# Optimization experiments

Measured on AMD Instinct MI355X. Metric: run time of the kernel, lower is better.

## Reference

```python
import jax, jax.numpy as jnp
import numpy as np


def setup_inputs() -> dict:
    key = jax.random.key(0)
    ks = jax.random.split(key, 7)
    B = 65536
    x = jax.random.normal(ks[0], (B, 1, 28, 28), dtype=jnp.float32)
    conv_w = jax.random.normal(ks[1], (4, 1, 7, 7), dtype=jnp.float32) * 0.1
    conv_b = jax.random.normal(ks[2], (4,), dtype=jnp.float32) * 0.1
    fc1_w = jax.random.normal(ks[3], (64, 256), dtype=jnp.float32) * 0.05
    fc1_b = jax.random.normal(ks[4], (64,), dtype=jnp.float32) * 0.05
    fc2_w = jax.random.normal(ks[5], (10, 64), dtype=jnp.float32) * 0.1
    fc2_b = jax.random.normal(ks[6], (10,), dtype=jnp.float32) * 0.1
    return {"x": x, "conv_w": conv_w, "conv_b": conv_b,
            "fc1_w": fc1_w, "fc1_b": fc1_b, "fc2_w": fc2_w, "fc2_b": fc2_b}


def reference(x, conv_w, conv_b, fc1_w, fc1_b, fc2_w, fc2_b):
    # conv1: 1->4 channels, 7x7 kernel, stride 3, no padding -> [B,4,8,8]
    h = jax.lax.conv_general_dilated(
        x, conv_w, window_strides=(3, 3), padding="VALID",
        dimension_numbers=("NCHW", "OIHW", "NCHW"))
    h = h + conv_b[None, :, None, None]
    h = h * h  # SquareFunction (CKKS polynomial activation)
    h = h.reshape(h.shape[0], -1)  # [B, 256]
    h = jnp.einsum("bi,oi->bo", h, fc1_w) + fc1_b
    h = h * h  # SquareFunction
    out = jnp.einsum("bi,oi->bo", h, fc2_w) + fc2_b  # [B, 10]
    return out
```

## Files before the change

### kernel.cpp

```cpp
#include <hip/hip_runtime.h>


#define BLK_IMGS    64
#define CHUNK_IMGS  16
#define NCHUNK      4
#define XCH_FLOATS  (CHUNK_IMGS * 784)
#define HB_PITCH    65

#define LDS_XBUF    0
#define LDS_H       12544
#define LDS_H2      29184
#define LDS_W2      33280
#define LDS_OUT     34304
#define LDS_TOTAL_F 34944

__global__ __launch_bounds__(1024)
void encconv_fused5(const float* __restrict__ x,
                    const float* __restrict__ conv_w,
                    const float* __restrict__ conv_b,
                    const float* __restrict__ fc1_w,
                    const float* __restrict__ fc1_b,
                    const float* __restrict__ fc2_w,
                    const float* __restrict__ fc2_b,
                    float* __restrict__ out)
{
    extern __shared__ float lds[];
    float*  xbuf = lds + LDS_XBUF;
    float4* hb   = (float4*)(lds + LDS_H);
    float4* h2b  = (float4*)(lds + LDS_H2);
    float4* w2b  = (float4*)(lds + LDS_W2);
    float*  ob   = lds + LDS_OUT;

    const int tid  = threadIdx.x;
    const int blk  = blockIdx.x;
    const long base_img = (long)blk * BLK_IMGS;

    const int lane = tid & 63;
    const int c    = __builtin_amdgcn_readfirstlane((tid >> 6) & 3);
    const int ghi  = __builtin_amdgcn_readfirstlane(tid >> 8);
    const int glo  = lane >> 4;
    const int y    = (lane >> 1) & 7;
    const int xh   = lane & 1;
    const int g    = ghi * 4 + glo;

    float ws[49];
    #pragma unroll
    for (int i = 0; i < 49; ++i) ws[i] = conv_w[c * 49 + i];
    const float cb = conv_b[c];

    if (tid < 160) {
        float4 v = *(const float4*)(fc2_w + tid * 4);
        int e  = tid * 4;
        int j  = e >> 6;
        int kk = (e & 63) >> 2;
        w2b[kk * 16 + j] = v;
    }

    const float* xblk = x + base_img * 784;

    float4 pf0, pf1, pf2, pf3;
    {
        const float* src = xblk;
        pf0 = *(const float4*)(src + 4 * tid);
        pf1 = *(const float4*)(src + 4 * (tid + 1024));
        pf2 = *(const float4*)(src + 4 * (tid + 2048));
        if (tid < 64) pf3 = *(const float4*)(src + 4 * (tid + 3072));
    }

    for (int ch = 0; ch < NCHUNK; ++ch) {
        *(float4*)(xbuf + 4 * tid)          = pf0;
        *(float4*)(xbuf + 4 * (tid + 1024)) = pf1;
        *(float4*)(xbuf + 4 * (tid + 2048)) = pf2;
        if (tid < 64) *(float4*)(xbuf + 4 * (tid + 3072)) = pf3;
        __syncthreads();

        if (ch + 1 < NCHUNK) {
            const float* src = xblk + (ch + 1) * XCH_FLOATS;
            pf0 = *(const float4*)(src + 4 * tid);
            pf1 = *(const float4*)(src + 4 * (tid + 1024));
            pf2 = *(const float4*)(src + 4 * (tid + 2048));
            if (tid < 64) pf3 = *(const float4*)(src + 4 * (tid + 3072));
        }

        float acc0 = 0.f, acc1 = 0.f, acc2 = 0.f, acc3 = 0.f;
        const float* xi = xbuf + g * 784;
        #pragma unroll
        for (int rr = 0; rr < 7; ++rr) {
            const float* rp = xi + (3 * y + rr) * 28 + 12 * xh;
            float4 r0 = *(const float4*)(rp + 0);
            float4 r1 = *(const float4*)(rp + 4);
            float4 r2 = *(const float4*)(rp + 8);
            float4 r3 = *(const float4*)(rp + 12);
            float r[16] = { r0.x, r0.y, r0.z, r0.w,
                            r1.x, r1.y, r1.z, r1.w,
                            r2.x, r2.y, r2.z, r2.w,
                            r3.x, r3.y, r3.z, r3.w };
            #pragma unroll
            for (int kx = 0; kx < 7; ++kx) {
                const float w = ws[rr * 7 + kx];
                acc0 = fmaf(r[0 + kx], w, acc0);
                acc1 = fmaf(r[3 + kx], w, acc1);
                acc2 = fmaf(r[6 + kx], w, acc2);
                acc3 = fmaf(r[9 + kx], w, acc3);
            }
        }

        float4 hv;
        hv.x = acc0 + cb; hv.x *= hv.x;
        hv.y = acc1 + cb; hv.y *= hv.y;
        hv.z = acc2 + cb; hv.z *= hv.z;
        hv.w = acc3 + cb; hv.w *= hv.w;
        hb[(c * 16 + y * 2 + xh) * HB_PITCH + (ch * CHUNK_IMGS + g)] = hv;

        __syncthreads();
    }

    {
        const int img = tid & 63;
        const int w4  = __builtin_amdgcn_readfirstlane(tid >> 6);
        const float* wbase = fc1_w + (w4 * 4) * 256;

        float a0 = 0.f, a1 = 0.f, a2 = 0.f, a3 = 0.f;

        #pragma unroll 4
        for (int k4 = 0; k4 < 64; ++k4) {
            float4 h4 = hb[k4 * HB_PITCH + img];
            const float* wp = wbase + k4 * 4;
            float4 w0 = *(const float4*)(wp + 0 * 256);
            float4 w1 = *(const float4*)(wp + 1 * 256);
            float4 w2 = *(const float4*)(wp + 2 * 256);
            float4 w3 = *(const float4*)(wp + 3 * 256);
            a0 = fmaf(h4.x,w0.x,a0); a0 = fmaf(h4.y,w0.y,a0); a0 = fmaf(h4.z,w0.z,a0); a0 = fmaf(h4.w,w0.w,a0);
            a1 = fmaf(h4.x,w1.x,a1); a1 = fmaf(h4.y,w1.y,a1); a1 = fmaf(h4.z,w1.z,a1); a1 = fmaf(h4.w,w1.w,a1);
            a2 = fmaf(h4.x,w2.x,a2); a2 = fmaf(h4.y,w2.y,a2); a2 = fmaf(h4.z,w2.z,a2); a2 = fmaf(h4.w,w2.w,a2);
            a3 = fmaf(h4.x,w3.x,a3); a3 = fmaf(h4.y,w3.y,a3); a3 = fmaf(h4.z,w3.z,a3); a3 = fmaf(h4.w,w3.w,a3);
        }

        const float* bp = fc1_b + w4 * 4;
        float4 p0;
        p0.x = a0 + bp[0]; p0.x *= p0.x;
        p0.y = a1 + bp[1]; p0.y *= p0.y;
        p0.z = a2 + bp[2]; p0.z *= p0.z;
        p0.w = a3 + bp[3]; p0.w *= p0.w;
        h2b[w4 * 64 + img] = p0;
    }
    __syncthreads();

    if (tid < 512) {
        const int im3 = tid >> 3;
        const int q   = tid & 7;

        float s1 = 0.f;
        #pragma unroll
        for (int k4 = 0; k4 < 16; ++k4) {
            float4 hh = h2b[k4 * 64 + im3];
            float4 wA = w2b[k4 * 16 + q];
            s1 = fmaf(hh.x, wA.x, s1); s1 = fmaf(hh.y, wA.y, s1);
            s1 = fmaf(hh.z, wA.z, s1); s1 = fmaf(hh.w, wA.w, s1);
        }
        ob[im3 * 10 + q] = s1 + fc2_b[q];

        if (q < 2) {
            float s2 = 0.f;
            #pragma unroll
            for (int k4 = 0; k4 < 16; ++k4) {
                float4 hh = h2b[k4 * 64 + im3];
                float4 wB = w2b[k4 * 16 + 8 + q];
                s2 = fmaf(hh.x, wB.x, s2); s2 = fmaf(hh.y, wB.y, s2);
                s2 = fmaf(hh.z, wB.z, s2); s2 = fmaf(hh.w, wB.w, s2);
            }
            ob[im3 * 10 + 8 + q] = s2 + fc2_b[8 + q];
        }
    }
    __syncthreads();

    if (tid < 160) {
        float4 v = *(const float4*)(ob + tid * 4);
        *(float4*)(out + (long)blk * 640 + tid * 4) = v;
    }
}

extern "C" void kernel_launch(void* const* d_in, const int* in_sizes, int n_in,
                              void* d_out, int out_size, void* d_ws, size_t ws_size,
                              hipStream_t stream) {
    const float* x      = (const float*)d_in[0];
    const float* conv_w = (const float*)d_in[1];
    const float* conv_b = (const float*)d_in[2];
    const float* fc1_w  = (const float*)d_in[3];
    const float* fc1_b  = (const float*)d_in[4];
    const float* fc2_w  = (const float*)d_in[5];
    const float* fc2_b  = (const float*)d_in[6];
    float* out = (float*)d_out;

    const int B = in_sizes[0] / 784;
    const int blocks = (B + BLK_IMGS - 1) / BLK_IMGS;
    const size_t lds_bytes = LDS_TOTAL_F * sizeof(float);

    static bool attr_set = false;
    if (!attr_set) {
        (void)hipFuncSetAttribute((const void*)encconv_fused5,
                                  hipFuncAttributeMaxDynamicSharedMemorySize,
                                  (int)lds_bytes);
        attr_set = true;
    }

    encconv_fused5<<<blocks, 1024, lds_bytes, stream>>>(
        x, conv_w, conv_b, fc1_w, fc1_b, fc2_w, fc2_b, out);
}
```

Baseline: 342.5 us.

## Interleave per-chunk fc1/fc2 with conv and use LDS atomics for fc2

FC1 and FC2 now run per 16-image chunk inside the chunk loop, overlapping the previous chunk's dense layers with the next chunk's LDS fill. FC2 is done by each thread atomically adding its hidden unit's contribution into LDS outputs pre-initialised with the bias. The h buffer shrinks to one chunk, which roughly halves LDS use and could allow two blocks per CU. The cost is 10 LDS float atomics per thread per chunk and more redundant global reads of fc1_w, and atomic ordering makes float summation nondeterministic.

```diff
diff --git a/kernel.cpp b/kernel.cpp
--- a/kernel.cpp
+++ b/kernel.cpp
@@ -5,17 +5,15 @@
 #define CHUNK_IMGS  16
 #define NCHUNK      4
 #define XCH_FLOATS  (CHUNK_IMGS * 784)
-#define HB_PITCH    65
+#define HB_PITCH    17
 
 #define LDS_XBUF    0
 #define LDS_H       12544
-#define LDS_H2      29184
-#define LDS_W2      33280
-#define LDS_OUT     34304
-#define LDS_TOTAL_F 34944
+#define LDS_OUT     16896
+#define LDS_TOTAL_F 17536
 
 __global__ __launch_bounds__(1024)
-void encconv_fused5(const float* __restrict__ x,
+void encconv_fused6(const float* __restrict__ x,
                     const float* __restrict__ conv_w,
                     const float* __restrict__ conv_b,
                     const float* __restrict__ fc1_w,
@@ -27,8 +25,6 @@
     extern __shared__ float lds[];
     float*  xbuf = lds + LDS_XBUF;
     float4* hb   = (float4*)(lds + LDS_H);
-    float4* h2b  = (float4*)(lds + LDS_H2);
-    float4* w2b  = (float4*)(lds + LDS_W2);
     float*  ob   = lds + LDS_OUT;
 
     const int tid  = threadIdx.x;
@@ -48,13 +44,11 @@
     for (int i = 0; i < 49; ++i) ws[i] = conv_w[c * 49 + i];
     const float cb = conv_b[c];
 
-    if (tid < 160) {
-        float4 v = *(const float4*)(fc2_w + tid * 4);
-        int e  = tid * 4;
-        int j  = e >> 6;
-        int kk = (e & 63) >> 2;
-        w2b[kk * 16 + j] = v;
-    }
+    const int o_sub = (tid >> 4) & 3;
+    const int img16 = tid & 15;
+    const int o     = ((tid >> 6) << 2) + o_sub;
+
+    if (tid < 640) ob[tid] = fc2_b[tid % 10];
 
     const float* xblk = x + base_img * 784;
 
@@ -67,11 +61,32 @@
         if (tid < 64) pf3 = *(const float4*)(src + 4 * (tid + 3072));
     }
 
+    auto fc1fc2 = [&](int ch) {
+        const float* wrow = fc1_w + o * 256;
+        float acc = 0.f;
+        #pragma unroll 4
+        for (int k4 = 0; k4 < 64; ++k4) {
+            float4 h4 = hb[k4 * HB_PITCH + img16];
+            float4 w4 = *(const float4*)(wrow + k4 * 4);
+            acc = fmaf(h4.x, w4.x, acc); acc = fmaf(h4.y, w4.y, acc);
+            acc = fmaf(h4.z, w4.z, acc); acc = fmaf(h4.w, w4.w, acc);
+        }
+        float t  = acc + fc1_b[o];
+        float h2 = t * t;
+        const int ig = ch * CHUNK_IMGS + img16;
+        #pragma unroll
+        for (int j = 0; j < 10; ++j) {
+            atomicAdd(ob + ig * 10 + j, h2 * fc2_w[j * 64 + o]);
+        }
+    };
+
     for (int ch = 0; ch < NCHUNK; ++ch) {
         *(float4*)(xbuf + 4 * tid)          = pf0;
         *(float4*)(xbuf + 4 * (tid + 1024)) = pf1;
         *(float4*)(xbuf + 4 * (tid + 2048)) = pf2;
         if (tid < 64) *(float4*)(xbuf + 4 * (tid + 3072)) = pf3;
+
+        if (ch > 0) fc1fc2(ch - 1);
         __syncthreads();
 
         if (ch + 1 < NCHUNK) {
@@ -110,68 +125,12 @@
         hv.y = acc1 + cb; hv.y *= hv.y;
         hv.z = acc2 + cb; hv.z *= hv.z;
         hv.w = acc3 + cb; hv.w *= hv.w;
-        hb[(c * 16 + y * 2 + xh) * HB_PITCH + (ch * CHUNK_IMGS + g)] = hv;
+        hb[(c * 16 + y * 2 + xh) * HB_PITCH + g] = hv;
 
         __syncthreads();
     }
 
-    {
-        const int img = tid & 63;
-        const int w4  = __builtin_amdgcn_readfirstlane(tid >> 6);
-        const float* wbase = fc1_w + (w4 * 4) * 256;
-
-        float a0 = 0.f, a1 = 0.f, a2 = 0.f, a3 = 0.f;
-
-        #pragma unroll 4
-        for (int k4 = 0; k4 < 64; ++k4) {
-            float4 h4 = hb[k4 * HB_PITCH + img];
-            const float* wp = wbase + k4 * 4;
-            float4 w0 = *(const float4*)(wp + 0 * 256);
-            float4 w1 = *(const float4*)(wp + 1 * 256);
-            float4 w2 = *(const float4*)(wp + 2 * 256);
-            float4 w3 = *(const float4*)(wp + 3 * 256);
-            a0 = fmaf(h4.x,w0.x,a0); a0 = fmaf(h4.y,w0.y,a0); a0 = fmaf(h4.z,w0.z,a0); a0 = fmaf(h4.w,w0.w,a0);
-            a1 = fmaf(h4.x,w1.x,a1); a1 = fmaf(h4.y,w1.y,a1); a1 = fmaf(h4.z,w1.z,a1); a1 = fmaf(h4.w,w1.w,a1);
-            a2 = fmaf(h4.x,w2.x,a2); a2 = fmaf(h4.y,w2.y,a2); a2 = fmaf(h4.z,w2.z,a2); a2 = fmaf(h4.w,w2.w,a2);
-            a3 = fmaf(h4.x,w3.x,a3); a3 = fmaf(h4.y,w3.y,a3); a3 = fmaf(h4.z,w3.z,a3); a3 = fmaf(h4.w,w3.w,a3);
-        }
-
-        const float* bp = fc1_b + w4 * 4;
-        float4 p0;
-        p0.x = a0 + bp[0]; p0.x *= p0.x;
-        p0.y = a1 + bp[1]; p0.y *= p0.y;
-        p0.z = a2 + bp[2]; p0.z *= p0.z;
-        p0.w = a3 + bp[3]; p0.w *= p0.w;
-        h2b[w4 * 64 + img] = p0;
-    }
-    __syncthreads();
-
-    if (tid < 512) {
-        const int im3 = tid >> 3;
-        const int q   = tid & 7;
-
-        float s1 = 0.f;
-        #pragma unroll
-        for (int k4 = 0; k4 < 16; ++k4) {
-            float4 hh = h2b[k4 * 64 + im3];
-            float4 wA = w2b[k4 * 16 + q];
-            s1 = fmaf(hh.x, wA.x, s1); s1 = fmaf(hh.y, wA.y, s1);
-            s1 = fmaf(hh.z, wA.z, s1); s1 = fmaf(hh.w, wA.w, s1);
-        }
-        ob[im3 * 10 + q] = s1 + fc2_b[q];
-
-        if (q < 2) {
-            float s2 = 0.f;
-            #pragma unroll
-            for (int k4 = 0; k4 < 16; ++k4) {
-                float4 hh = h2b[k4 * 64 + im3];
-                float4 wB = w2b[k4 * 16 + 8 + q];
-                s2 = fmaf(hh.x, wB.x, s2); s2 = fmaf(hh.y, wB.y, s2);
-                s2 = fmaf(hh.z, wB.z, s2); s2 = fmaf(hh.w, wB.w, s2);
-            }
-            ob[im3 * 10 + 8 + q] = s2 + fc2_b[8 + q];
-        }
-    }
+    fc1fc2(NCHUNK - 1);
     __syncthreads();
 
     if (tid < 160) {
@@ -198,12 +157,12 @@
 
     static bool attr_set = false;
     if (!attr_set) {
-        (void)hipFuncSetAttribute((const void*)encconv_fused5,
+        (void)hipFuncSetAttribute((const void*)encconv_fused6,
                                   hipFuncAttributeMaxDynamicSharedMemorySize,
                                   (int)lds_bytes);
         attr_set = true;
     }
 
-    encconv_fused5<<<blocks, 1024, lds_bytes, stream>>>(
+    encconv_fused6<<<blocks, 1024, lds_bytes, stream>>>(
         x, conv_w, conv_b, fc1_w, fc1_b, fc2_w, fc2_b, out);
 }
```

Result: slower. 613.7 us (+79.2%).

## Read conv input directly from global, drop LDS staging and chunk loop

Applied to the files above, without the earlier changes.

The convolution stage now reads each image's rows straight from global memory into registers. Each thread computes four output rows by reusing every loaded input row across the overlapping kernel windows, which replaces the chunked LDS staging with prefetch and its per-chunk barriers. The fc2 stage now has one wavefront per output class reading fc2 weights from global, and it writes the output directly instead of through LDS. LDS use drops, which could allow more resident blocks, but the global input loads are strided per thread and less coalesced, and the output stores are scattered.

```diff
diff --git a/kernel.cpp b/kernel.cpp
--- a/kernel.cpp
+++ b/kernel.cpp
@@ -1,21 +1,12 @@
 #include <hip/hip_runtime.h>
 
 
-#define BLK_IMGS    64
-#define CHUNK_IMGS  16
-#define NCHUNK      4
-#define XCH_FLOATS  (CHUNK_IMGS * 784)
-#define HB_PITCH    65
-
-#define LDS_XBUF    0
-#define LDS_H       12544
-#define LDS_H2      29184
-#define LDS_W2      33280
-#define LDS_OUT     34304
-#define LDS_TOTAL_F 34944
+#define BLK_IMGS  64
+#define LDS_H2    16384
+#define LDS_TOTAL_F 20480
 
 __global__ __launch_bounds__(1024)
-void encconv_fused5(const float* __restrict__ x,
+void encconv_fused7(const float* __restrict__ x,
                     const float* __restrict__ conv_w,
                     const float* __restrict__ conv_b,
                     const float* __restrict__ fc1_w,
@@ -25,106 +16,82 @@
                     float* __restrict__ out)
 {
     extern __shared__ float lds[];
-    float*  xbuf = lds + LDS_XBUF;
-    float4* hb   = (float4*)(lds + LDS_H);
-    float4* h2b  = (float4*)(lds + LDS_H2);
-    float4* w2b  = (float4*)(lds + LDS_W2);
-    float*  ob   = lds + LDS_OUT;
+    float4* hb  = (float4*)lds;
+    float4* h2b = (float4*)(lds + LDS_H2);
 
     const int tid  = threadIdx.x;
     const int blk  = blockIdx.x;
     const long base_img = (long)blk * BLK_IMGS;
 
+    const int w    = tid >> 6;
     const int lane = tid & 63;
-    const int c    = __builtin_amdgcn_readfirstlane((tid >> 6) & 3);
-    const int ghi  = __builtin_amdgcn_readfirstlane(tid >> 8);
-    const int glo  = lane >> 4;
-    const int y    = (lane >> 1) & 7;
-    const int xh   = lane & 1;
-    const int g    = ghi * 4 + glo;
+
+    const int c     = __builtin_amdgcn_readfirstlane(w >> 2);
+    const int imgHi = __builtin_amdgcn_readfirstlane(w & 3);
+    const int imgLo = lane >> 2;
+    const int yh    = (lane >> 1) & 1;
+    const int xh    = lane & 1;
+    const int img   = imgHi * 16 + imgLo;
 
     float ws[49];
     #pragma unroll
     for (int i = 0; i < 49; ++i) ws[i] = conv_w[c * 49 + i];
     const float cb = conv_b[c];
 
-    if (tid < 160) {
-        float4 v = *(const float4*)(fc2_w + tid * 4);
-        int e  = tid * 4;
-        int j  = e >> 6;
-        int kk = (e & 63) >> 2;
-        w2b[kk * 16 + j] = v;
+    float4 acc[4];
+    #pragma unroll
+    for (int yy = 0; yy < 4; ++yy) acc[yy] = make_float4(0.f, 0.f, 0.f, 0.f);
+
+    const float* xi = x + (base_img + img) * 784 + yh * 12 * 28 + 12 * xh;
+    #pragma unroll
+    for (int rw = 0; rw < 16; ++rw) {
+        const float* rp = xi + rw * 28;
+        float4 r0 = *(const float4*)(rp + 0);
+        float4 r1 = *(const float4*)(rp + 4);
+        float4 r2 = *(const float4*)(rp + 8);
+        float4 r3 = *(const float4*)(rp + 12);
+        float r[16] = { r0.x, r0.y, r0.z, r0.w,
+                        r1.x, r1.y, r1.z, r1.w,
+                        r2.x, r2.y, r2.z, r2.w,
+                        r3.x, r3.y, r3.z, r3.w };
+        #pragma unroll
+        for (int yy = 0; yy < 4; ++yy) {
+            const int rr = rw - 3 * yy;
+            if (rr >= 0 && rr <= 6) {
+                #pragma unroll
+                for (int kx = 0; kx < 7; ++kx) {
+                    const float wv = ws[rr * 7 + kx];
+                    acc[yy].x = fmaf(r[0 + kx], wv, acc[yy].x);
+                    acc[yy].y = fmaf(r[3 + kx], wv, acc[yy].y);
+                    acc[yy].z = fmaf(r[6 + kx], wv, acc[yy].z);
+                    acc[yy].w = fmaf(r[9 + kx], wv, acc[yy].w);
+                }
+            }
+        }
     }
 
-    const float* xblk = x + base_img * 784;
-
-    float4 pf0, pf1, pf2, pf3;
-    {
-        const float* src = xblk;
-        pf0 = *(const float4*)(src + 4 * tid);
-        pf1 = *(const float4*)(src + 4 * (tid + 1024));
-        pf2 = *(const float4*)(src + 4 * (tid + 2048));
-        if (tid < 64) pf3 = *(const float4*)(src + 4 * (tid + 3072));
+    #pragma unroll
+    for (int yy = 0; yy < 4; ++yy) {
+        float4 hv;
+        hv.x = acc[yy].x + cb; hv.x *= hv.x;
+        hv.y = acc[yy].y + cb; hv.y *= hv.y;
+        hv.z = acc[yy].z + cb; hv.z *= hv.z;
+        hv.w = acc[yy].w + cb; hv.w *= hv.w;
+        const int k4 = c * 16 + (yh * 4 + yy) * 2 + xh;
+        hb[k4 * 64 + img] = hv;
     }
-
-    for (int ch = 0; ch < NCHUNK; ++ch) {
-        *(float4*)(xbuf + 4 * tid)          = pf0;
-        *(float4*)(xbuf + 4 * (tid + 1024)) = pf1;
-        *(float4*)(xbuf + 4 * (tid + 2048)) = pf2;
-        if (tid < 64) *(float4*)(xbuf + 4 * (tid + 3072)) = pf3;
-        __syncthreads();
-
-        if (ch + 1 < NCHUNK) {
-            const float* src = xblk + (ch + 1) * XCH_FLOATS;
-            pf0 = *(const float4*)(src + 4 * tid);
-            pf1 = *(const float4*)(src + 4 * (tid + 1024));
-            pf2 = *(const float4*)(src + 4 * (tid + 2048));
-            if (tid < 64) pf3 = *(const float4*)(src + 4 * (tid + 3072));
-        }
-
-        float acc0 = 0.f, acc1 = 0.f, acc2 = 0.f, acc3 = 0.f;
-        const float* xi = xbuf + g * 784;
-        #pragma unroll
-        for (int rr = 0; rr < 7; ++rr) {
-            const float* rp = xi + (3 * y + rr) * 28 + 12 * xh;
-            float4 r0 = *(const float4*)(rp + 0);
-            float4 r1 = *(const float4*)(rp + 4);
-            float4 r2 = *(const float4*)(rp + 8);
-            float4 r3 = *(const float4*)(rp + 12);
-            float r[16] = { r0.x, r0.y, r0.z, r0.w,
-                            r1.x, r1.y, r1.z, r1.w,
-                            r2.x, r2.y, r2.z, r2.w,
-                            r3.x, r3.y, r3.z, r3.w };
-            #pragma unroll
-            for (int kx = 0; kx < 7; ++kx) {
-                const float w = ws[rr * 7 + kx];
-                acc0 = fmaf(r[0 + kx], w, acc0);
-                acc1 = fmaf(r[3 + kx], w, acc1);
-                acc2 = fmaf(r[6 + kx], w, acc2);
-                acc3 = fmaf(r[9 + kx], w, acc3);
-            }
-        }
-
-        float4 hv;
-        hv.x = acc0 + cb; hv.x *= hv.x;
-        hv.y = acc1 + cb; hv.y *= hv.y;
-        hv.z = acc2 + cb; hv.z *= hv.z;
-        hv.w = acc3 + cb; hv.w *= hv.w;
-        hb[(c * 16 + y * 2 + xh) * HB_PITCH + (ch * CHUNK_IMGS + g)] = hv;
-
-        __syncthreads();
-    }
+    __syncthreads();
 
     {
-        const int img = tid & 63;
-        const int w4  = __builtin_amdgcn_readfirstlane(tid >> 6);
+        const int img64 = lane;
+        const int w4    = __builtin_amdgcn_readfirstlane(w);
         const float* wbase = fc1_w + (w4 * 4) * 256;
 
         float a0 = 0.f, a1 = 0.f, a2 = 0.f, a3 = 0.f;
 
         #pragma unroll 4
         for (int k4 = 0; k4 < 64; ++k4) {
-            float4 h4 = hb[k4 * HB_PITCH + img];
+            float4 h4 = hb[k4 * 64 + img64];
             const float* wp = wbase + k4 * 4;
             float4 w0 = *(const float4*)(wp + 0 * 256);
             float4 w1 = *(const float4*)(wp + 1 * 256);
@@ -142,41 +109,21 @@
         p0.y = a1 + bp[1]; p0.y *= p0.y;
         p0.z = a2 + bp[2]; p0.z *= p0.z;
         p0.w = a3 + bp[3]; p0.w *= p0.w;
-        h2b[w4 * 64 + img] = p0;
+        h2b[w4 * 64 + img64] = p0;
     }
     __syncthreads();
 
-    if (tid < 512) {
-        const int im3 = tid >> 3;
-        const int q   = tid & 7;
-
-        float s1 = 0.f;
+    if (w < 10) {
+        const int j = __builtin_amdgcn_readfirstlane(w);
+        float s = 0.f;
         #pragma unroll
         for (int k4 = 0; k4 < 16; ++k4) {
-            float4 hh = h2b[k4 * 64 + im3];
-            float4 wA = w2b[k4 * 16 + q];
-            s1 = fmaf(hh.x, wA.x, s1); s1 = fmaf(hh.y, wA.y, s1);
-            s1 = fmaf(hh.z, wA.z, s1); s1 = fmaf(hh.w, wA.w, s1);
+            float4 hh = h2b[k4 * 64 + lane];
+            float4 wj = *(const float4*)(fc2_w + j * 64 + k4 * 4);
+            s = fmaf(hh.x, wj.x, s); s = fmaf(hh.y, wj.y, s);
+            s = fmaf(hh.z, wj.z, s); s = fmaf(hh.w, wj.w, s);
         }
-        ob[im3 * 10 + q] = s1 + fc2_b[q];
-
-        if (q < 2) {
-            float s2 = 0.f;
-            #pragma unroll
-            for (int k4 = 0; k4 < 16; ++k4) {
-                float4 hh = h2b[k4 * 64 + im3];
-                float4 wB = w2b[k4 * 16 + 8 + q];
-                s2 = fmaf(hh.x, wB.x, s2); s2 = fmaf(hh.y, wB.y, s2);
-                s2 = fmaf(hh.z, wB.z, s2); s2 = fmaf(hh.w, wB.w, s2);
-            }
-            ob[im3 * 10 + 8 + q] = s2 + fc2_b[8 + q];
-        }
-    }
-    __syncthreads();
-
-    if (tid < 160) {
-        float4 v = *(const float4*)(ob + tid * 4);
-        *(float4*)(out + (long)blk * 640 + tid * 4) = v;
+        out[(long)blk * 640 + lane * 10 + j] = s + fc2_b[j];
     }
 }
 
@@ -198,12 +145,12 @@
 
     static bool attr_set = false;
     if (!attr_set) {
-        (void)hipFuncSetAttribute((const void*)encconv_fused5,
+        (void)hipFuncSetAttribute((const void*)encconv_fused7,
                                   hipFuncAttributeMaxDynamicSharedMemorySize,
                                   (int)lds_bytes);
         attr_set = true;
     }
 
-    encconv_fused5<<<blocks, 1024, lds_bytes, stream>>>(
+    encconv_fused7<<<blocks, 1024, lds_bytes, stream>>>(
         x, conv_w, conv_b, fc1_w, fc1_b, fc2_w, fc2_b, out);
 }
```

Result: slower. 446.3 us (+30.3%).

## Halve block to 32 images and 512 threads, remap fc1/fc2 work per wave

Applied to the files above, without the earlier changes.

Shrinks each block to 32 images with 512 threads and half the LDS, so more and smaller blocks can be resident per CU and barrier stalls affect fewer waves. The fc1 stage now has each wave compute 8 output neurons for 32 images, with the two half-waves selecting different output quads. Each lane therefore loads twice as many fc1 weights per k step and holds 8 accumulators. fc2 is remapped to 16 lanes per image with 10 active. Register pressure rises and the redundant half-wave weight loads double global/L1 weight traffic in fc1.

```diff
diff --git a/kernel.cpp b/kernel.cpp
--- a/kernel.cpp
+++ b/kernel.cpp
@@ -1,21 +1,22 @@
 #include <hip/hip_runtime.h>
 
 
-#define BLK_IMGS    64
-#define CHUNK_IMGS  16
+#define BLK_IMGS    32
+#define CHUNK_IMGS  8
 #define NCHUNK      4
 #define XCH_FLOATS  (CHUNK_IMGS * 784)
-#define HB_PITCH    65
+#define HB_PITCH    33
+#define H2_PITCH    33
 
 #define LDS_XBUF    0
-#define LDS_H       12544
-#define LDS_H2      29184
-#define LDS_W2      33280
-#define LDS_OUT     34304
-#define LDS_TOTAL_F 34944
-
-__global__ __launch_bounds__(1024)
-void encconv_fused5(const float* __restrict__ x,
+#define LDS_H       6272
+#define LDS_H2      14720
+#define LDS_W2      16832
+#define LDS_OUT     17856
+#define LDS_TOTAL_F 18176
+
+__global__ __launch_bounds__(512)
+void encconv_fused8(const float* __restrict__ x,
                     const float* __restrict__ conv_w,
                     const float* __restrict__ conv_b,
                     const float* __restrict__ fc1_w,
@@ -36,8 +37,10 @@
     const long base_img = (long)blk * BLK_IMGS;
 
     const int lane = tid & 63;
-    const int c    = __builtin_amdgcn_readfirstlane((tid >> 6) & 3);
-    const int ghi  = __builtin_amdgcn_readfirstlane(tid >> 8);
+    const int wv   = tid >> 6;
+
+    const int c    = __builtin_amdgcn_readfirstlane(wv >> 1);
+    const int ghi  = __builtin_amdgcn_readfirstlane(wv & 1);
     const int glo  = lane >> 4;
     const int y    = (lane >> 1) & 7;
     const int xh   = lane & 1;
@@ -62,24 +65,24 @@
     {
         const float* src = xblk;
         pf0 = *(const float4*)(src + 4 * tid);
-        pf1 = *(const float4*)(src + 4 * (tid + 1024));
-        pf2 = *(const float4*)(src + 4 * (tid + 2048));
-        if (tid < 64) pf3 = *(const float4*)(src + 4 * (tid + 3072));
+        pf1 = *(const float4*)(src + 4 * (tid + 512));
+        pf2 = *(const float4*)(src + 4 * (tid + 1024));
+        if (tid < 32) pf3 = *(const float4*)(src + 4 * (tid + 1536));
     }
 
     for (int ch = 0; ch < NCHUNK; ++ch) {
         *(float4*)(xbuf + 4 * tid)          = pf0;
-        *(float4*)(xbuf + 4 * (tid + 1024)) = pf1;
-        *(float4*)(xbuf + 4 * (tid + 2048)) = pf2;
-        if (tid < 64) *(float4*)(xbuf + 4 * (tid + 3072)) = pf3;
+        *(float4*)(xbuf + 4 * (tid + 512))  = pf1;
+        *(float4*)(xbuf + 4 * (tid + 1024)) = pf2;
+        if (tid < 32) *(float4*)(xbuf + 4 * (tid + 1536)) = pf3;
         __syncthreads();
 
         if (ch + 1 < NCHUNK) {
             const float* src = xblk + (ch + 1) * XCH_FLOATS;
             pf0 = *(const float4*)(src + 4 * tid);
-            pf1 = *(const float4*)(src + 4 * (tid + 1024));
-            pf2 = *(const float4*)(src + 4 * (tid + 2048));
-            if (tid < 64) pf3 = *(const float4*)(src + 4 * (tid + 3072));
+            pf1 = *(const float4*)(src + 4 * (tid + 512));
+            pf2 = *(const float4*)(src + 4 * (tid + 1024));
+            if (tid < 32) pf3 = *(const float4*)(src + 4 * (tid + 1536));
         }
 
         float acc0 = 0.f, acc1 = 0.f, acc2 = 0.f, acc3 = 0.f;
@@ -116,13 +119,14 @@
     }
 
     {
-        const int img = tid & 63;
-        const int w4  = __builtin_amdgcn_readfirstlane(tid >> 6);
-        const float* wbase = fc1_w + (w4 * 4) * 256;
-
-        float a0 = 0.f, a1 = 0.f, a2 = 0.f, a3 = 0.f;
-
-        #pragma unroll 4
+        const int img = lane & 31;
+        const int oh  = lane >> 5;
+        const int w8  = __builtin_amdgcn_readfirstlane(wv);
+        const float* wbase = fc1_w + (w8 * 8) * 256;
+
+        float a0=0.f,a1=0.f,a2=0.f,a3=0.f,a4=0.f,a5=0.f,a6=0.f,a7=0.f;
+
+        #pragma unroll 2
         for (int k4 = 0; k4 < 64; ++k4) {
             float4 h4 = hb[k4 * HB_PITCH + img];
             const float* wp = wbase + k4 * 4;
@@ -130,53 +134,54 @@
             float4 w1 = *(const float4*)(wp + 1 * 256);
             float4 w2 = *(const float4*)(wp + 2 * 256);
             float4 w3 = *(const float4*)(wp + 3 * 256);
+            float4 w4 = *(const float4*)(wp + 4 * 256);
+            float4 w5 = *(const float4*)(wp + 5 * 256);
+            float4 w6 = *(const float4*)(wp + 6 * 256);
+            float4 w7 = *(const float4*)(wp + 7 * 256);
             a0 = fmaf(h4.x,w0.x,a0); a0 = fmaf(h4.y,w0.y,a0); a0 = fmaf(h4.z,w0.z,a0); a0 = fmaf(h4.w,w0.w,a0);
             a1 = fmaf(h4.x,w1.x,a1); a1 = fmaf(h4.y,w1.y,a1); a1 = fmaf(h4.z,w1.z,a1); a1 = fmaf(h4.w,w1.w,a1);
             a2 = fmaf(h4.x,w2.x,a2); a2 = fmaf(h4.y,w2.y,a2); a2 = fmaf(h4.z,w2.z,a2); a2 = fmaf(h4.w,w2.w,a2);
             a3 = fmaf(h4.x,w3.x,a3); a3 = fmaf(h4.y,w3.y,a3); a3 = fmaf(h4.z,w3.z,a3); a3 = fmaf(h4.w,w3.w,a3);
-        }
-
-        const float* bp = fc1_b + w4 * 4;
+            a4 = fmaf(h4.x,w4.x,a4); a4 = fmaf(h4.y,w4.y,a4); a4 = fmaf(h4.z,w4.z,a4); a4 = fmaf(h4.w,w4.w,a4);
+            a5 = fmaf(h4.x,w5.x,a5); a5 = fmaf(h4.y,w5.y,a5); a5 = fmaf(h4.z,w5.z,a5); a5 = fmaf(h4.w,w5.w,a5);
+            a6 = fmaf(h4.x,w6.x,a6); a6 = fmaf(h4.y,w6.y,a6); a6 = fmaf(h4.z,w6.z,a6); a6 = fmaf(h4.w,w6.w,a6);
+            a7 = fmaf(h4.x,w7.x,a7); a7 = fmaf(h4.y,w7.y,a7); a7 = fmaf(h4.z,w7.z,a7); a7 = fmaf(h4.w,w7.w,a7);
+        }
+
+        const float* bp = fc1_b + w8 * 8;
+        float s0 = oh ? a4 : a0;  float b0 = oh ? bp[4] : bp[0];
+        float s1 = oh ? a5 : a1;  float b1 = oh ? bp[5] : bp[1];
+        float s2 = oh ? a6 : a2;  float b2 = oh ? bp[6] : bp[2];
+        float s3 = oh ? a7 : a3;  float b3 = oh ? bp[7] : bp[3];
         float4 p0;
-        p0.x = a0 + bp[0]; p0.x *= p0.x;
-        p0.y = a1 + bp[1]; p0.y *= p0.y;
-        p0.z = a2 + bp[2]; p0.z *= p0.z;
-        p0.w = a3 + bp[3]; p0.w *= p0.w;
-        h2b[w4 * 64 + img] = p0;
+        p0.x = s0 + b0; p0.x *= p0.x;
+        p0.y = s1 + b1; p0.y *= p0.y;
+        p0.z = s2 + b2; p0.z *= p0.z;
+        p0.w = s3 + b3; p0.w *= p0.w;
+        h2b[(w8 * 2 + oh) * H2_PITCH + img] = p0;
     }
     __syncthreads();
 
-    if (tid < 512) {
-        const int im3 = tid >> 3;
-        const int q   = tid & 7;
-
-        float s1 = 0.f;
-        #pragma unroll
-        for (int k4 = 0; k4 < 16; ++k4) {
-            float4 hh = h2b[k4 * 64 + im3];
-            float4 wA = w2b[k4 * 16 + q];
-            s1 = fmaf(hh.x, wA.x, s1); s1 = fmaf(hh.y, wA.y, s1);
-            s1 = fmaf(hh.z, wA.z, s1); s1 = fmaf(hh.w, wA.w, s1);
-        }
-        ob[im3 * 10 + q] = s1 + fc2_b[q];
-
-        if (q < 2) {
-            float s2 = 0.f;
+    {
+        const int im5 = tid >> 4;
+        const int q   = tid & 15;
+        if (q < 10) {
+            float s = 0.f;
             #pragma unroll
             for (int k4 = 0; k4 < 16; ++k4) {
-                float4 hh = h2b[k4 * 64 + im3];
-                float4 wB = w2b[k4 * 16 + 8 + q];
-                s2 = fmaf(hh.x, wB.x, s2); s2 = fmaf(hh.y, wB.y, s2);
-                s2 = fmaf(hh.z, wB.z, s2); s2 = fmaf(hh.w, wB.w, s2);
+                float4 hh = h2b[k4 * H2_PITCH + im5];
+                float4 wA = w2b[k4 * 16 + q];
+                s = fmaf(hh.x, wA.x, s); s = fmaf(hh.y, wA.y, s);
+                s = fmaf(hh.z, wA.z, s); s = fmaf(hh.w, wA.w, s);
             }
-            ob[im3 * 10 + 8 + q] = s2 + fc2_b[8 + q];
+            ob[im5 * 10 + q] = s + fc2_b[q];
         }
     }
     __syncthreads();
 
-    if (tid < 160) {
+    if (tid < 80) {
         float4 v = *(const float4*)(ob + tid * 4);
-        *(float4*)(out + (long)blk * 640 + tid * 4) = v;
+        *(float4*)(out + (long)blk * 320 + tid * 4) = v;
     }
 }
 
@@ -198,12 +203,12 @@
 
     static bool attr_set = false;
     if (!attr_set) {
-        (void)hipFuncSetAttribute((const void*)encconv_fused5,
+        (void)hipFuncSetAttribute((const void*)encconv_fused8,
                                   hipFuncAttributeMaxDynamicSharedMemorySize,
                                   (int)lds_bytes);
         attr_set = true;
     }
 
-    encconv_fused5<<<blocks, 1024, lds_bytes, stream>>>(
+    encconv_fused8<<<blocks, 512, lds_bytes, stream>>>(
         x, conv_w, conv_b, fc1_w, fc1_b, fc2_w, fc2_b, out);
 }
```

New measurement: 344.2 us. About the same (+0.5%).
